# Performance work log

Hardware: AMD Instinct MI355X
Metric: run time of the kernel (lower is better)

## Reference

```python
import jax, jax.numpy as jnp
import numpy as np

EPS = 1e-6

def _ln(x, w, b):
    m = x.mean(-1, keepdims=True)
    v = ((x - m) ** 2).mean(-1, keepdims=True)
    return (x - m) / jnp.sqrt(v + EPS) * w + b

def setup_inputs() -> dict:
    key = jax.random.key(0)
    ks = jax.random.split(key, 16)
    N, P, C, M = 8192, 64, 128, 4096
    MW = M * P  # 262144 gathered tokens
    A, BL = 131072, 65536
    x = jax.random.normal(ks[0], (N, P, C), dtype=jnp.float32)
    index_window = jax.random.permutation(ks[1], N)[:M]
    index_partition = jax.random.permutation(ks[2], MW)
    perm2 = jax.random.permutation(ks[3], MW)
    asy_index = perm2[:A]
    blocked_index = perm2[A:A + BL]
    p = lambda k, sh: 0.02 * jax.random.normal(k, sh, dtype=jnp.float32)
    return {
        "x": x,
        "index_window": index_window,
        "index_partition": index_partition,
        "asy_index": asy_index,
        "blocked_index": blocked_index,
        "M": M,
        "B": N,
        "ln1_w": jnp.ones((C,), jnp.float32), "ln1_b": jnp.zeros((C,), jnp.float32),
        "qkv_w": p(ks[4], (C, 3 * C)), "qkv_b": jnp.zeros((3 * C,), jnp.float32),
        "proj_w": p(ks[5], (C, C)), "proj_b": jnp.zeros((C,), jnp.float32),
        "gamma1": jnp.full((C,), 1e-1, jnp.float32),
        "ln2_w": jnp.ones((C,), jnp.float32), "ln2_b": jnp.zeros((C,), jnp.float32),
        "mlp_w1": p(ks[6], (C, 4 * C)), "mlp_b1": jnp.zeros((4 * C,), jnp.float32),
        "mlp_w2": p(ks[7], (4 * C, C)), "mlp_b2": jnp.zeros((C,), jnp.float32),
        "gamma2": jnp.full((C,), 1e-1, jnp.float32),
    }

def reference(x, index_window, index_partition, asy_index, blocked_index, M, B,
              ln1_w, ln1_b, qkv_w, qkv_b, proj_w, proj_b, gamma1,
              ln2_w, ln2_b, mlp_w1, mlp_b1, mlp_w2, mlp_b2, gamma2):
    N, P, C = x.shape
    H, dh = 4, 32
    scale = dh ** -0.5
    MW = index_partition.shape[0]
    x = _ln(x, ln1_w, ln1_b)                      # first_norm over whole input
    X = x                                          # (N, P, C)
    xw = x[index_window].reshape(-1, C)            # gather windows -> (MW, C)
    XX = xw
    xa = _ln(xw[asy_index], ln1_w, ln1_b)          # second norm on asy tokens
    xw = xw.at[asy_index].set(xa)
    shortcut = xa                                  # (A, C)
    xp = xw[index_partition].reshape(M, -1, C)     # (M, P, C) attention groups
    qkv = (xp @ qkv_w + qkv_b).reshape(M, P, H, 3 * dh).transpose(0, 2, 1, 3)
    q, k, v = jnp.split(qkv, 3, axis=3)            # each (M, H, P, dh)
    attn = jnp.einsum('mhqd,mhkd->mhqk', q, k) * scale
    # scatter scores keyed by key-token into flat map, mask blocked keys, gather back
    am = jnp.zeros((MW, P, H), attn.dtype)
    am = am.at[index_partition].set(jnp.transpose(attn, (0, 3, 2, 1)).reshape(MW, P, H))
    am = am.at[blocked_index].set(-10000.0)
    attn = jnp.transpose(am[index_partition].reshape(M, P, P, H), (0, 3, 2, 1))
    attn = jax.nn.softmax(attn, axis=-1)
    o = jnp.einsum('mhqk,mhkd->mhqd', attn, v).transpose(0, 2, 1, 3).reshape(M, P, C)
    o = o @ proj_w + proj_b
    XX = XX.at[index_partition].set(o.reshape(-1, C))
    y = XX[asy_index]
    # sub_layers: [ls1, droppath(id), ln2, mlp, ls2, droppath(id)]
    y = y * gamma1                                 # i=0
    y = shortcut + y                               # i=1 residual
    shortcut = y
    y2 = _ln(y, ln2_w, ln2_b)                      # i=2
    y2 = jax.nn.gelu(y2 @ mlp_w1 + mlp_b1, approximate=False) @ mlp_w2 + mlp_b2  # i=3
    y2 = y2 * gamma2                               # i=4
    y = shortcut + y2                              # i=5 residual
    XX = XX.at[asy_index].set(y)
    XX = XX.at[blocked_index].set(X[index_window].reshape(-1, C)[blocked_index])
    X = X.at[index_window].set(XX.reshape(M, -1, C))
    return X
```

## Files before the change

kernel.cpp:

```cpp
#include <hip/hip_runtime.h>
#include <hip/hip_bf16.h>
#include <math.h>

#define N_   8192
#define P_   64
#define C_   128
#define M_   4096
#define MW_  (M_ * P_)
#define A_   131072
#define BL_  65536
#define NROWS_ (N_ * P_)

typedef __attribute__((ext_vector_type(8))) __bf16 bf16x8;
typedef __attribute__((ext_vector_type(4))) float f32x4;
typedef __attribute__((ext_vector_type(2))) __bf16 bf16x2;

__device__ __forceinline__ float wave_sum(float v) {
#pragma unroll
  for (int o = 32; o > 0; o >>= 1) v += __shfl_xor(v, o, 64);
  return v;
}

__global__ __launch_bounds__(256) void k_set8(unsigned char* p, int n) {
  int i = blockIdx.x * 256 + threadIdx.x;
  if (i < n) p[i] = 0;
}
__global__ __launch_bounds__(256) void k_scatter2(unsigned char* p,
                                                  const int* __restrict__ ia,
                                                  const int* __restrict__ ib) {
  int i = blockIdx.x * 256 + threadIdx.x;
  if (i < A_) p[ia[i]] = 1;
  else {
    int j = i - A_;
    if (j < BL_) p[ib[j]] = 2;
  }
}

__global__ __launch_bounds__(256) void k_prep(const float* __restrict__ qkvw,
                                              const float* __restrict__ projw,
                                              const float* __restrict__ w1,
                                              const float* __restrict__ w2,
                                              __bf16* __restrict__ qkvt,
                                              __bf16* __restrict__ projt,
                                              __bf16* __restrict__ w1t,
                                              __bf16* __restrict__ w2t) {
  int i = blockIdx.x * 256 + threadIdx.x;
  if (i < 384 * 128) {
    int col = i >> 7, row = i & 127;
    qkvt[i] = (__bf16)qkvw[row * 384 + col];
  } else if (i < 384 * 128 + 128 * 128) {
    int j = i - 384 * 128;
    int col = j >> 7, row = j & 127;
    projt[j] = (__bf16)projw[row * 128 + col];
  } else if (i < 384 * 128 + 128 * 128 + 512 * 128) {
    int j = i - 384 * 128 - 128 * 128;
    int col = j >> 7, row = j & 127;
    w1t[j] = (__bf16)w1[row * 512 + col];
  } else {
    int j = i - 384 * 128 - 128 * 128 - 512 * 128;
    int col = j >> 9, row = j & 511;
    w2t[j] = (__bf16)w2[row * 128 + col];
  }
}

__global__ __launch_bounds__(256) void k_ln_all(const float* __restrict__ x,
                                                const float* __restrict__ w,
                                                const float* __restrict__ b,
                                                float* __restrict__ out) {
  int row = blockIdx.x * 4 + (threadIdx.x >> 6);
  int lane = threadIdx.x & 63;
  float2 xv = ((const float2*)(x + (size_t)row * 128))[lane];
  float mean = wave_sum(xv.x + xv.y) * (1.0f / 128.0f);
  float d0 = xv.x - mean, d1 = xv.y - mean;
  float inv = rsqrtf(wave_sum(d0 * d0 + d1 * d1) * (1.0f / 128.0f) + 1e-6f);
  float2 wv = ((const float2*)w)[lane];
  float2 bv = ((const float2*)b)[lane];
  float2 o2;
  o2.x = d0 * inv * wv.x + bv.x;
  o2.y = d1 * inv * wv.y + bv.y;
  ((float2*)(out + (size_t)row * 128))[lane] = o2;
}

__global__ __launch_bounds__(256, 3) void k_attn(
    const int* __restrict__ iw,
    const int* __restrict__ ip, const unsigned char* __restrict__ flags,
    const float* __restrict__ ln1w, const float* __restrict__ ln1b,
    const __bf16* __restrict__ qkvt, const float* __restrict__ qkvb,
    const __bf16* __restrict__ projt, const float* __restrict__ projb,
    float* out) {
  __shared__ __align__(16) __bf16 XV[64 * 132];
  __shared__ __align__(16) __bf16 scratch[4 * 4352];
  __shared__ int srow[64];
  __shared__ unsigned char fl[64];

  const int tid = threadIdx.x;
  const int w = tid >> 6, lane = tid & 63;
  const int quad = lane >> 4, cl = lane & 15;
  const int m = blockIdx.x;

  if (tid < 64) {
    int s = ip[(m << 6) + tid];
    fl[tid] = flags[s];
    srow[tid] = iw[s >> 6] * 64 + (s & 63);
  }
  __syncthreads();

  __bf16* Xs = XV;
  const float lw0 = ln1w[2 * lane], lw1 = ln1w[2 * lane + 1];
  const float lb0 = ln1b[2 * lane], lb1 = ln1b[2 * lane + 1];

  for (int half = 0; half < 2; ++half) {
    float2 xv[8];
#pragma unroll
    for (int ii = 0; ii < 8; ++ii) {
      int r = w + 4 * (half * 8 + ii);
      xv[ii] = ((const float2*)(out + (size_t)srow[r] * 128))[lane];
    }
#pragma unroll
    for (int ii = 0; ii < 8; ++ii) {
      int r = w + 4 * (half * 8 + ii);
      float y0 = xv[ii].x, y1 = xv[ii].y;
      if (fl[r] == 1) {
        float mean = wave_sum(y0 + y1) * (1.0f / 128.0f);
        float d0 = y0 - mean, d1 = y1 - mean;
        float inv = rsqrtf(wave_sum(d0 * d0 + d1 * d1) * (1.0f / 128.0f) + 1e-6f);
        y0 = d0 * inv * lw0 + lb0;
        y1 = d1 * inv * lw1 + lb1;
      }
      bf16x2 p2;
      p2[0] = (__bf16)y0; p2[1] = (__bf16)y1;
      *(bf16x2*)&Xs[r * 132 + 2 * lane] = p2;
    }
  }
  __syncthreads();

  __bf16* wsc = scratch + w * 4352;
  __bf16* Qs  = wsc;
  __bf16* Ks  = wsc + 2176;
  __bf16* Vts = XV + w * 2112;
  __bf16* Ps  = wsc;
  __bf16* Os  = wsc;
  const int h = w;

  bf16x8 af[4][4];
#pragma unroll
  for (int mt = 0; mt < 4; ++mt)
#pragma unroll
    for (int kt = 0; kt < 4; ++kt)
      af[mt][kt] = *(const bf16x8*)&Xs[(mt * 16 + cl) * 132 + kt * 32 + quad * 8];
  __syncthreads();

#pragma unroll
  for (int t = 0; t < 3; ++t) {
#pragma unroll
    for (int nt = 0; nt < 2; ++nt) {
      int col = h * 96 + t * 32 + nt * 16 + cl;
      bf16x8 bfr[4];
#pragma unroll
      for (int kt = 0; kt < 4; ++kt)
        bfr[kt] = *(const bf16x8*)&qkvt[(size_t)col * 128 + kt * 32 + quad * 8];
      float bias = qkvb[col];
      __builtin_amdgcn_s_setprio(1);
#pragma unroll
      for (int mt = 0; mt < 4; ++mt) {
        f32x4 acc = {bias, bias, bias, bias};
#pragma unroll
        for (int kt = 0; kt < 4; ++kt)
          acc = __builtin_amdgcn_mfma_f32_16x16x32_bf16(af[mt][kt], bfr[kt], acc, 0, 0, 0);
        if (t == 0) {
#pragma unroll
          for (int r = 0; r < 4; ++r)
            Qs[(mt * 16 + quad * 4 + r) * 34 + nt * 16 + cl] = (__bf16)acc[r];
        } else if (t == 1) {
#pragma unroll
          for (int r = 0; r < 4; ++r)
            Ks[(mt * 16 + quad * 4 + r) * 34 + nt * 16 + cl] = (__bf16)acc[r];
        } else {
#pragma unroll
          for (int r = 0; r < 4; ++r)
            Vts[(nt * 16 + cl) * 66 + mt * 16 + quad * 4 + r] = (__bf16)acc[r];
        }
      }
      __builtin_amdgcn_s_setprio(0);
    }
  }

  f32x4 sc4[4][4];
  {
    bf16x8 bk[4];
#pragma unroll
    for (int nt = 0; nt < 4; ++nt)
      bk[nt] = *(const bf16x8*)&Ks[(nt * 16 + cl) * 34 + quad * 8];
    __builtin_amdgcn_s_setprio(1);
#pragma unroll
    for (int mt = 0; mt < 4; ++mt) {
      bf16x8 aq = *(const bf16x8*)&Qs[(mt * 16 + cl) * 34 + quad * 8];
#pragma unroll
      for (int nt = 0; nt < 4; ++nt) {
        f32x4 z = {0.f, 0.f, 0.f, 0.f};
        sc4[mt][nt] = __builtin_amdgcn_mfma_f32_16x16x32_bf16(aq, bk[nt], z, 0, 0, 0);
      }
    }
    __builtin_amdgcn_s_setprio(0);
  }
  const float scale = 0.17677669529663687f;
  bool blk[4];
#pragma unroll
  for (int nt = 0; nt < 4; ++nt) blk[nt] = (fl[nt * 16 + cl] == 2);
#pragma unroll
  for (int mt = 0; mt < 4; ++mt)
#pragma unroll
    for (int nt = 0; nt < 4; ++nt)
#pragma unroll
      for (int r = 0; r < 4; ++r) {
        float v = sc4[mt][nt][r];
        sc4[mt][nt][r] = blk[nt] ? -10000.0f : v * scale;
      }
#pragma unroll
  for (int mt = 0; mt < 4; ++mt) {
#pragma unroll
    for (int r = 0; r < 4; ++r) {
      float mx = fmaxf(fmaxf(sc4[mt][0][r], sc4[mt][1][r]),
                       fmaxf(sc4[mt][2][r], sc4[mt][3][r]));
#pragma unroll
      for (int off = 1; off < 16; off <<= 1) mx = fmaxf(mx, __shfl_xor(mx, off, 64));
      float e0 = __expf(sc4[mt][0][r] - mx);
      float e1 = __expf(sc4[mt][1][r] - mx);
      float e2 = __expf(sc4[mt][2][r] - mx);
      float e3 = __expf(sc4[mt][3][r] - mx);
      float sm = (e0 + e1) + (e2 + e3);
#pragma unroll
      for (int off = 1; off < 16; off <<= 1) sm += __shfl_xor(sm, off, 64);
      float inv = 1.0f / sm;
      int row = mt * 16 + quad * 4 + r;
      Ps[row * 68 +  0 + cl] = (__bf16)(e0 * inv);
      Ps[row * 68 + 16 + cl] = (__bf16)(e1 * inv);
      Ps[row * 68 + 32 + cl] = (__bf16)(e2 * inv);
      Ps[row * 68 + 48 + cl] = (__bf16)(e3 * inv);
    }
  }

  f32x4 oacc[4][2];
  {
    bf16x8 bv[2][2];
#pragma unroll
    for (int nt = 0; nt < 2; ++nt)
#pragma unroll
      for (int kt = 0; kt < 2; ++kt)
        bv[nt][kt] = *(const bf16x8*)&Vts[(nt * 16 + cl) * 66 + kt * 32 + quad * 8];
    __builtin_amdgcn_s_setprio(1);
#pragma unroll
    for (int mt = 0; mt < 4; ++mt) {
      bf16x8 ap0 = *(const bf16x8*)&Ps[(mt * 16 + cl) * 68 + quad * 8];
      bf16x8 ap1 = *(const bf16x8*)&Ps[(mt * 16 + cl) * 68 + 32 + quad * 8];
#pragma unroll
      for (int nt = 0; nt < 2; ++nt) {
        f32x4 z = {0.f, 0.f, 0.f, 0.f};
        z = __builtin_amdgcn_mfma_f32_16x16x32_bf16(ap0, bv[nt][0], z, 0, 0, 0);
        z = __builtin_amdgcn_mfma_f32_16x16x32_bf16(ap1, bv[nt][1], z, 0, 0, 0);
        oacc[mt][nt] = z;
      }
    }
    __builtin_amdgcn_s_setprio(0);
  }
#pragma unroll
  for (int mt = 0; mt < 4; ++mt)
#pragma unroll
    for (int nt = 0; nt < 2; ++nt)
#pragma unroll
      for (int r = 0; r < 4; ++r)
        Os[(mt * 16 + quad * 4 + r) * 36 + nt * 16 + cl] = (__bf16)oacc[mt][nt][r];
  __syncthreads();

  const int jw = w * 32;
#pragma unroll
  for (int mt = 0; mt < 4; ++mt) {
#pragma unroll
    for (int nt = 0; nt < 2; ++nt) {
      int col = jw + nt * 16 + cl;
      float pb = projb[col];
      f32x4 acc = {pb, pb, pb, pb};
#pragma unroll
      for (int kt = 0; kt < 4; ++kt) {
        const __bf16* op = scratch + kt * 4352;
        bf16x8 a = *(const bf16x8*)&op[(mt * 16 + cl) * 36 + quad * 8];
        bf16x8 bb = *(const bf16x8*)&projt[(size_t)col * 128 + kt * 32 + quad * 8];
        acc = __builtin_amdgcn_mfma_f32_16x16x32_bf16(a, bb, acc, 0, 0, 0);
      }
#pragma unroll
      for (int r = 0; r < 4; ++r) {
        int row = mt * 16 + quad * 4 + r;
        if (fl[row] != 2)
          out[(size_t)srow[row] * 128 + col] = acc[r];
      }
    }
  }
}

__global__ __launch_bounds__(256, 3) void k_mlp(
    const float* __restrict__ x, const int* __restrict__ iw,
    const int* __restrict__ ia,
    const float* __restrict__ ln1w, const float* __restrict__ ln1b,
    const float* __restrict__ g1,
    const float* __restrict__ ln2w, const float* __restrict__ ln2b,
    const __bf16* __restrict__ w1t, const float* __restrict__ b1,
    const __bf16* __restrict__ w2t, const float* __restrict__ b2,
    const float* __restrict__ g2,
    float* __restrict__ out) {
  __shared__ __align__(16) float ys[64][130];
  __shared__ __align__(16) __bf16 buf[64 * 132];
  __shared__ int wrs[64];

  const int tid = threadIdx.x;
  const int w = tid >> 6, lane = tid & 63;
  const int quad = lane >> 4, cl = lane & 15;

  if (tid < 64) {
    int s = ia[(blockIdx.x << 6) + tid];
    wrs[tid] = iw[s >> 6] * 64 + (s & 63);
  }
  __syncthreads();

  const float lw0 = ln1w[2 * lane], lw1 = ln1w[2 * lane + 1];
  const float lb0 = ln1b[2 * lane], lb1 = ln1b[2 * lane + 1];
  const float g1a = g1[2 * lane], g1b = g1[2 * lane + 1];
  const float l2w0 = ln2w[2 * lane], l2w1 = ln2w[2 * lane + 1];
  const float l2b0 = ln2b[2 * lane], l2b1 = ln2b[2 * lane + 1];

  for (int half = 0; half < 2; ++half) {
    float2 xv[8], ov[8];
#pragma unroll
    for (int ii = 0; ii < 8; ++ii) {
      int r = w + 4 * (half * 8 + ii);
      size_t wr = (size_t)wrs[r];
      xv[ii] = ((const float2*)(x + wr * 128))[lane];
      ov[ii] = ((const float2*)(out + wr * 128))[lane];
    }
#pragma unroll
    for (int ii = 0; ii < 8; ++ii) {
      int r = w + 4 * (half * 8 + ii);
      float mean = wave_sum(xv[ii].x + xv[ii].y) * (1.0f / 128.0f);
      float d0 = xv[ii].x - mean, d1 = xv[ii].y - mean;
      float inv = rsqrtf(wave_sum(d0 * d0 + d1 * d1) * (1.0f / 128.0f) + 1e-6f);
      float y0 = d0 * inv * lw0 + lb0, y1 = d1 * inv * lw1 + lb1;
      mean = wave_sum(y0 + y1) * (1.0f / 128.0f);
      d0 = y0 - mean; d1 = y1 - mean;
      inv = rsqrtf(wave_sum(d0 * d0 + d1 * d1) * (1.0f / 128.0f) + 1e-6f);
      float xa0 = d0 * inv * lw0 + lb0, xa1 = d1 * inv * lw1 + lb1;
      float yv0 = xa0 + g1a * ov[ii].x;
      float yv1 = xa1 + g1b * ov[ii].y;
      ys[r][2 * lane] = yv0;
      ys[r][2 * lane + 1] = yv1;
      mean = wave_sum(yv0 + yv1) * (1.0f / 128.0f);
      d0 = yv0 - mean; d1 = yv1 - mean;
      inv = rsqrtf(wave_sum(d0 * d0 + d1 * d1) * (1.0f / 128.0f) + 1e-6f);
      bf16x2 p2;
      p2[0] = (__bf16)(d0 * inv * l2w0 + l2b0);
      p2[1] = (__bf16)(d1 * inv * l2w1 + l2b1);
      *(bf16x2*)&buf[r * 132 + 2 * lane] = p2;
    }
  }
  __syncthreads();

  bf16x8 af[4][4];
#pragma unroll
  for (int mt = 0; mt < 4; ++mt)
#pragma unroll
    for (int kt = 0; kt < 4; ++kt)
      af[mt][kt] = *(const bf16x8*)&buf[(mt * 16 + cl) * 132 + kt * 32 + quad * 8];
  __syncthreads();

  f32x4 zacc[4][2];
#pragma unroll
  for (int nt = 0; nt < 2; ++nt) {
    float bb = b2[w * 32 + nt * 16 + cl];
#pragma unroll
    for (int mt = 0; mt < 4; ++mt) zacc[mt][nt] = (f32x4){bb, bb, bb, bb};
  }

  for (int ch = 0; ch < 4; ++ch) {
#pragma unroll
    for (int nt = 0; nt < 2; ++nt) {
      int col = ch * 128 + w * 32 + nt * 16 + cl;
      bf16x8 bfr[4];
#pragma unroll
      for (int kt = 0; kt < 4; ++kt)
        bfr[kt] = *(const bf16x8*)&w1t[(size_t)col * 128 + kt * 32 + quad * 8];
      float bias = b1[col];
      __builtin_amdgcn_s_setprio(1);
#pragma unroll
      for (int mt = 0; mt < 4; ++mt) {
        f32x4 acc = {bias, bias, bias, bias};
#pragma unroll
        for (int kt = 0; kt < 4; ++kt)
          acc = __builtin_amdgcn_mfma_f32_16x16x32_bf16(af[mt][kt], bfr[kt], acc, 0, 0, 0);
#pragma unroll
        for (int r = 0; r < 4; ++r) {
          float a = acc[r];
          float g = a * 0.5f * (1.0f + erff(a * 0.70710678118654752f));
          buf[(mt * 16 + quad * 4 + r) * 132 + w * 32 + nt * 16 + cl] = (__bf16)g;
        }
      }
      __builtin_amdgcn_s_setprio(0);
    }
    __syncthreads();
    bf16x8 ah[4][4];
#pragma unroll
    for (int mt = 0; mt < 4; ++mt)
#pragma unroll
      for (int kk = 0; kk < 4; ++kk)
        ah[mt][kk] = *(const bf16x8*)&buf[(mt * 16 + cl) * 132 + kk * 32 + quad * 8];
#pragma unroll
    for (int nt = 0; nt < 2; ++nt) {
      int col = w * 32 + nt * 16 + cl;
      bf16x8 bfr[4];
#pragma unroll
      for (int kk = 0; kk < 4; ++kk)
        bfr[kk] = *(const bf16x8*)&w2t[(size_t)col * 512 + ch * 128 + kk * 32 + quad * 8];
      __builtin_amdgcn_s_setprio(1);
#pragma unroll
      for (int mt = 0; mt < 4; ++mt)
#pragma unroll
        for (int kk = 0; kk < 4; ++kk)
          zacc[mt][nt] = __builtin_amdgcn_mfma_f32_16x16x32_bf16(ah[mt][kk], bfr[kk],
                                                                 zacc[mt][nt], 0, 0, 0);
      __builtin_amdgcn_s_setprio(0);
    }
    __syncthreads();
  }

#pragma unroll
  for (int mt = 0; mt < 4; ++mt)
#pragma unroll
    for (int nt = 0; nt < 2; ++nt) {
      int col = w * 32 + nt * 16 + cl;
      float gg = g2[col];
#pragma unroll
      for (int r = 0; r < 4; ++r) {
        int row = mt * 16 + quad * 4 + r;
        out[(size_t)wrs[row] * 128 + col] = ys[row][col] + gg * zacc[mt][nt][r];
      }
    }
}

extern "C" void kernel_launch(void* const* d_in, const int* in_sizes, int n_in,
                              void* d_out, int out_size, void* d_ws, size_t ws_size,
                              hipStream_t stream) {
  const float* x = (const float*)d_in[0];
  const int* iw = (const int*)d_in[1];
  const int* ip = (const int*)d_in[2];
  const int* ia = (const int*)d_in[3];
  const int* ib = (const int*)d_in[4];
  const float* ln1w = (const float*)d_in[7];
  const float* ln1b = (const float*)d_in[8];
  const float* qkvw = (const float*)d_in[9];
  const float* qkvb = (const float*)d_in[10];
  const float* projw = (const float*)d_in[11];
  const float* projb = (const float*)d_in[12];
  const float* g1 = (const float*)d_in[13];
  const float* ln2w = (const float*)d_in[14];
  const float* ln2b = (const float*)d_in[15];
  const float* w1 = (const float*)d_in[16];
  const float* b1 = (const float*)d_in[17];
  const float* w2 = (const float*)d_in[18];
  const float* b2 = (const float*)d_in[19];
  const float* g2 = (const float*)d_in[20];
  float* out = (float*)d_out;

  unsigned char* flags = (unsigned char*)d_ws;
  __bf16* qkvt = (__bf16*)((char*)d_ws + MW_);
  __bf16* projt = (__bf16*)((char*)d_ws + MW_ + 384 * 128 * 2);
  __bf16* w1t = (__bf16*)((char*)d_ws + MW_ + 384 * 128 * 2 + 128 * 128 * 2);
  __bf16* w2t = (__bf16*)((char*)d_ws + MW_ + 384 * 128 * 2 + 128 * 128 * 2 + 512 * 128 * 2);

  k_set8<<<MW_ / 256, 256, 0, stream>>>(flags, MW_);
  k_scatter2<<<(A_ + BL_) / 256, 256, 0, stream>>>(flags, ia, ib);
  k_prep<<<(384 * 128 + 128 * 128 + 512 * 128 + 128 * 512) / 256, 256, 0, stream>>>(
      qkvw, projw, w1, w2, qkvt, projt, w1t, w2t);
  k_ln_all<<<NROWS_ / 4, 256, 0, stream>>>(x, ln1w, ln1b, out);
  k_attn<<<M_, 256, 0, stream>>>(iw, ip, flags, ln1w, ln1b, qkvt, qkvb,
                                 projt, projb, out);
  k_mlp<<<A_ / 64, 256, 0, stream>>>(x, iw, ia, ln1w, ln1b, g1, ln2w, ln2b,
                                     w1t, b1, w2t, b2, g2, out);
}
```

Measured before the change: 881.3 us.

## Vectorize LayerNorm, widen attn gather, slim MLP shared memory for occupancy

```diff
diff --git a/kernel.cpp b/kernel.cpp
--- a/kernel.cpp
+++ b/kernel.cpp
@@ -67,18 +67,26 @@
                                                 const float* __restrict__ w,
                                                 const float* __restrict__ b,
                                                 float* __restrict__ out) {
-  int row = blockIdx.x * 4 + (threadIdx.x >> 6);
-  int lane = threadIdx.x & 63;
-  float2 xv = ((const float2*)(x + (size_t)row * 128))[lane];
-  float mean = wave_sum(xv.x + xv.y) * (1.0f / 128.0f);
-  float d0 = xv.x - mean, d1 = xv.y - mean;
-  float inv = rsqrtf(wave_sum(d0 * d0 + d1 * d1) * (1.0f / 128.0f) + 1e-6f);
-  float2 wv = ((const float2*)w)[lane];
-  float2 bv = ((const float2*)b)[lane];
-  float2 o2;
-  o2.x = d0 * inv * wv.x + bv.x;
-  o2.y = d1 * inv * wv.y + bv.y;
-  ((float2*)(out + (size_t)row * 128))[lane] = o2;
+  int hw = threadIdx.x >> 5, l = threadIdx.x & 31;
+  size_t row = (size_t)blockIdx.x * 8 + hw;
+  float4 v = ((const float4*)(x + row * 128))[l];
+  float s = (v.x + v.y) + (v.z + v.w);
+#pragma unroll
+  for (int o = 1; o < 32; o <<= 1) s += __shfl_xor(s, o, 64);
+  float mean = s * (1.0f / 128.0f);
+  float d0 = v.x - mean, d1 = v.y - mean, d2 = v.z - mean, d3 = v.w - mean;
+  float q = (d0 * d0 + d1 * d1) + (d2 * d2 + d3 * d3);
+#pragma unroll
+  for (int o = 1; o < 32; o <<= 1) q += __shfl_xor(q, o, 64);
+  float inv = rsqrtf(q * (1.0f / 128.0f) + 1e-6f);
+  float4 wv = ((const float4*)w)[l];
+  float4 bv = ((const float4*)b)[l];
+  float4 o4;
+  o4.x = d0 * inv * wv.x + bv.x;
+  o4.y = d1 * inv * wv.y + bv.y;
+  o4.z = d2 * inv * wv.z + bv.z;
+  o4.w = d3 * inv * wv.w + bv.w;
+  ((float4*)(out + row * 128))[l] = o4;
 }
 
 __global__ __launch_bounds__(256, 3) void k_attn(
@@ -109,16 +117,16 @@
   const float lw0 = ln1w[2 * lane], lw1 = ln1w[2 * lane + 1];
   const float lb0 = ln1b[2 * lane], lb1 = ln1b[2 * lane + 1];
 
-  for (int half = 0; half < 2; ++half) {
-    float2 xv[8];
-#pragma unroll
-    for (int ii = 0; ii < 8; ++ii) {
-      int r = w + 4 * (half * 8 + ii);
+  {
+    float2 xv[16];
+#pragma unroll
+    for (int ii = 0; ii < 16; ++ii) {
+      int r = w + 4 * ii;
       xv[ii] = ((const float2*)(out + (size_t)srow[r] * 128))[lane];
     }
 #pragma unroll
-    for (int ii = 0; ii < 8; ++ii) {
-      int r = w + 4 * (half * 8 + ii);
+    for (int ii = 0; ii < 16; ++ii) {
+      int r = w + 4 * ii;
       float y0 = xv[ii].x, y1 = xv[ii].y;
       if (fl[r] == 1) {
         float mean = wave_sum(y0 + y1) * (1.0f / 128.0f);
@@ -297,7 +305,7 @@
   }
 }
 
-__global__ __launch_bounds__(256, 3) void k_mlp(
+__global__ __launch_bounds__(256, 4) void k_mlp(
     const float* __restrict__ x, const int* __restrict__ iw,
     const int* __restrict__ ia,
     const float* __restrict__ ln1w, const float* __restrict__ ln1b,
@@ -306,9 +314,9 @@
     const __bf16* __restrict__ w1t, const float* __restrict__ b1,
     const __bf16* __restrict__ w2t, const float* __restrict__ b2,
     const float* __restrict__ g2,
-    float* __restrict__ out) {
-  __shared__ __align__(16) float ys[64][130];
-  __shared__ __align__(16) __bf16 buf[64 * 132];
+    float* out) {
+  __shared__ __align__(16) __bf16 y2s[64 * 136];
+  __shared__ __align__(16) __bf16 hb[64 * 136];
   __shared__ int wrs[64];
 
   const int tid = threadIdx.x;
@@ -349,25 +357,17 @@
       float xa0 = d0 * inv * lw0 + lb0, xa1 = d1 * inv * lw1 + lb1;
       float yv0 = xa0 + g1a * ov[ii].x;
       float yv1 = xa1 + g1b * ov[ii].y;
-      ys[r][2 * lane] = yv0;
-      ys[r][2 * lane + 1] = yv1;
+      ((float2*)(out + (size_t)wrs[r] * 128))[lane] = make_float2(yv0, yv1);
       mean = wave_sum(yv0 + yv1) * (1.0f / 128.0f);
       d0 = yv0 - mean; d1 = yv1 - mean;
       inv = rsqrtf(wave_sum(d0 * d0 + d1 * d1) * (1.0f / 128.0f) + 1e-6f);
       bf16x2 p2;
       p2[0] = (__bf16)(d0 * inv * l2w0 + l2b0);
       p2[1] = (__bf16)(d1 * inv * l2w1 + l2b1);
-      *(bf16x2*)&buf[r * 132 + 2 * lane] = p2;
-    }
-  }
-  __syncthreads();
-
-  bf16x8 af[4][4];
-#pragma unroll
-  for (int mt = 0; mt < 4; ++mt)
-#pragma unroll
-    for (int kt = 0; kt < 4; ++kt)
-      af[mt][kt] = *(const bf16x8*)&buf[(mt * 16 + cl) * 132 + kt * 32 + quad * 8];
+      *(bf16x2*)&y2s[r * 136 + 2 * lane] = p2;
+    }
+  }
+  __threadfence_block();
   __syncthreads();
 
   f32x4 zacc[4][2];
@@ -392,24 +392,20 @@
       for (int mt = 0; mt < 4; ++mt) {
         f32x4 acc = {bias, bias, bias, bias};
 #pragma unroll
-        for (int kt = 0; kt < 4; ++kt)
-          acc = __builtin_amdgcn_mfma_f32_16x16x32_bf16(af[mt][kt], bfr[kt], acc, 0, 0, 0);
+        for (int kt = 0; kt < 4; ++kt) {
+          bf16x8 a = *(const bf16x8*)&y2s[(mt * 16 + cl) * 136 + kt * 32 + quad * 8];
+          acc = __builtin_amdgcn_mfma_f32_16x16x32_bf16(a, bfr[kt], acc, 0, 0, 0);
+        }
 #pragma unroll
         for (int r = 0; r < 4; ++r) {
           float a = acc[r];
           float g = a * 0.5f * (1.0f + erff(a * 0.70710678118654752f));
-          buf[(mt * 16 + quad * 4 + r) * 132 + w * 32 + nt * 16 + cl] = (__bf16)g;
+          hb[(mt * 16 + quad * 4 + r) * 136 + w * 32 + nt * 16 + cl] = (__bf16)g;
         }
       }
       __builtin_amdgcn_s_setprio(0);
     }
     __syncthreads();
-    bf16x8 ah[4][4];
-#pragma unroll
-    for (int mt = 0; mt < 4; ++mt)
-#pragma unroll
-      for (int kk = 0; kk < 4; ++kk)
-        ah[mt][kk] = *(const bf16x8*)&buf[(mt * 16 + cl) * 132 + kk * 32 + quad * 8];
 #pragma unroll
     for (int nt = 0; nt < 2; ++nt) {
       int col = w * 32 + nt * 16 + cl;
@@ -421,9 +417,11 @@
 #pragma unroll
       for (int mt = 0; mt < 4; ++mt)
 #pragma unroll
-        for (int kk = 0; kk < 4; ++kk)
-          zacc[mt][nt] = __builtin_amdgcn_mfma_f32_16x16x32_bf16(ah[mt][kk], bfr[kk],
-                                                                 zacc[mt][nt], 0, 0, 0);
+        for (int kk = 0; kk < 4; ++kk) {
+          bf16x8 a = *(const bf16x8*)&hb[(mt * 16 + cl) * 136 + kk * 32 + quad * 8];
+          zacc[mt][nt] = __builtin_amdgcn_mfma_f32_16x16x32_bf16(a, bfr[kk],
+                                                                zacc[mt][nt], 0, 0, 0);
+        }
       __builtin_amdgcn_s_setprio(0);
     }
     __syncthreads();
@@ -438,7 +436,8 @@
 #pragma unroll
       for (int r = 0; r < 4; ++r) {
         int row = mt * 16 + quad * 4 + r;
-        out[(size_t)wrs[row] * 128 + col] = ys[row][col] + gg * zacc[mt][nt][r];
+        size_t a = (size_t)wrs[row] * 128 + col;
+        out[a] = out[a] + gg * zacc[mt][nt][r];
       }
     }
 }
@@ -477,7 +476,7 @@
   k_scatter2<<<(A_ + BL_) / 256, 256, 0, stream>>>(flags, ia, ib);
   k_prep<<<(384 * 128 + 128 * 128 + 512 * 128 + 128 * 512) / 256, 256, 0, stream>>>(
       qkvw, projw, w1, w2, qkvt, projt, w1t, w2t);
-  k_ln_all<<<NROWS_ / 4, 256, 0, stream>>>(x, ln1w, ln1b, out);
+  k_ln_all<<<NROWS_ / 8, 256, 0, stream>>>(x, ln1w, ln1b, out);
   k_attn<<<M_, 256, 0, stream>>>(iw, ip, flags, ln1w, ln1b, qkvt, qkvb,
                                  projt, projb, out);
   k_mlp<<<A_ / 64, 256, 0, stream>>>(x, iw, ia, ln1w, ln1b, g1, ln2w, ln2b,
```

Result: faster. 804.3 us (-8.7%).
